# Kernel tuning notes

Measured on AMD Instinct MI355X. Metric: run time of the kernel, lower is better.

The kernel has to match this reference:

```python
import jax, jax.numpy as jnp
import numpy as np

B, N, D, S, ITERS, EPS = 32, 4096, 512, 8, 3, 1e-8


def layer_norm(x, g, b, eps=1e-5):
    mu = jnp.mean(x, axis=-1, keepdims=True)
    var = jnp.var(x, axis=-1, keepdims=True)
    return (x - mu) * jax.lax.rsqrt(var + eps) * g + b


def setup_inputs() -> dict:
    key = jax.random.key(0)
    ks = jax.random.split(key, 12)
    sc = 1.0 / np.sqrt(D)
    return {
        "inputs": jax.random.normal(ks[0], (B, N, D), jnp.float32),
        "noise": jax.random.normal(ks[1], (B, S, D), jnp.float32),
        "slots_mu": jax.random.normal(ks[2], (1, S, D), jnp.float32),
        "slots_sigma": jnp.ones((1, S, D), jnp.float32),
        "ln_in_g": jnp.ones((D,), jnp.float32), "ln_in_b": jnp.zeros((D,), jnp.float32),
        "ln_s_g": jnp.ones((D,), jnp.float32), "ln_s_b": jnp.zeros((D,), jnp.float32),
        "wq": jax.random.normal(ks[3], (D, D), jnp.float32) * sc,
        "wk": jax.random.normal(ks[4], (D, D), jnp.float32) * sc,
        "wv": jax.random.normal(ks[5], (D, D), jnp.float32) * sc,
        "w_ih": jax.random.normal(ks[6], (3 * D, D), jnp.float32) * sc,
        "w_hh": jax.random.normal(ks[7], (3 * D, D), jnp.float32) * sc,
        "b_ih": jnp.zeros((3 * D,), jnp.float32),
        "b_hh": jnp.zeros((3 * D,), jnp.float32),
        "ln_m_g": jnp.ones((D,), jnp.float32), "ln_m_b": jnp.zeros((D,), jnp.float32),
        "w1": jax.random.normal(ks[8], (D, D), jnp.float32) * sc,
        "b1": jnp.zeros((D,), jnp.float32),
        "w2": jax.random.normal(ks[9], (D, D), jnp.float32) * sc,
        "b2": jnp.zeros((D,), jnp.float32),
    }


def reference(inputs, noise, slots_mu, slots_sigma, ln_in_g, ln_in_b, ln_s_g, ln_s_b,
              wq, wk, wv, w_ih, w_hh, b_ih, b_hh, ln_m_g, ln_m_b, w1, b1, w2, b2):
    # slot init: mu + sigma * N(0,1)
    slots = slots_mu + slots_sigma * noise          # (B,S,D)
    x = layer_norm(inputs, ln_in_g, ln_in_b)        # (B,N,D)
    k = jnp.einsum('bnd,ed->bne', x, wk)            # (B,N,D)
    v = jnp.einsum('bnd,ed->bne', x, wv)            # (B,N,D)
    for _ in range(ITERS):
        slots_prev = slots
        sn = layer_norm(slots, ln_s_g, ln_s_b)
        q = jnp.einsum('bsd,ed->bse', sn, wq)       # (B,S,D)
        logits = jnp.einsum('bnd,bsd->bns', k, q)   # (B,N,S)
        attn = jax.nn.softmax(logits, axis=-1) + EPS  # softmax over slots
        attn = attn / jnp.sum(attn, axis=-1, keepdims=True)
        attn_t = jnp.swapaxes(attn, -1, -2)         # (B,S,N)
        updates = jnp.einsum('bsn,bnd->bsd', attn_t, v)
        # GRUCell(input=updates, hidden=slots_prev)
        gi = jnp.einsum('bsd,ed->bse', updates, w_ih) + b_ih
        gh = jnp.einsum('bsd,ed->bse', slots_prev, w_hh) + b_hh
        gi_r, gi_z, gi_n = jnp.split(gi, 3, axis=-1)
        gh_r, gh_z, gh_n = jnp.split(gh, 3, axis=-1)
        r = jax.nn.sigmoid(gi_r + gh_r)
        z = jax.nn.sigmoid(gi_z + gh_z)
        n = jnp.tanh(gi_n + r * gh_n)
        slots = (1.0 - z) * n + z * slots_prev
        # residual MLP
        h = layer_norm(slots, ln_m_g, ln_m_b)
        h = jax.nn.relu(jnp.einsum('bsd,ed->bse', h, w1) + b1)
        slots = slots + jnp.einsum('bsd,ed->bse', h, w2) + b2
    return slots
```

## Files before the change

### kernel.cpp

```cpp
#include <hip/hip_runtime.h>

#define B_ 32
#define N_ 4096
#define D_ 512
#define S_ 8
#define ITERS_ 3
#define CH 32
#define RPC (N_/CH)

__device__ __forceinline__ float sigmoid_f(float x) {
    return 1.0f / (1.0f + __expf(-x));
}
__device__ __forceinline__ float tanh_f(float x) {
    float e = __expf(2.0f * x);
    return 1.0f - 2.0f / (e + 1.0f);
}

__global__ __launch_bounds__(256) void k_init(const float* __restrict__ noise,
                                              const float* __restrict__ mu,
                                              const float* __restrict__ sg,
                                              float* __restrict__ slots,
                                              float* __restrict__ stats) {
    int wid = threadIdx.x >> 6, lane = threadIdx.x & 63;
    int row = blockIdx.x * 4 + wid;
    const float4* nz = (const float4*)(noise + (size_t)row * D_);
    const float4* m4 = (const float4*)(mu + (size_t)(row & 7) * D_);
    const float4* s4 = (const float4*)(sg + (size_t)(row & 7) * D_);
    float4 v0 = nz[lane], v1 = nz[64 + lane];
    float4 a0 = m4[lane], a1 = m4[64 + lane];
    float4 c0 = s4[lane], c1 = s4[64 + lane];
    v0.x = fmaf(c0.x, v0.x, a0.x); v0.y = fmaf(c0.y, v0.y, a0.y);
    v0.z = fmaf(c0.z, v0.z, a0.z); v0.w = fmaf(c0.w, v0.w, a0.w);
    v1.x = fmaf(c1.x, v1.x, a1.x); v1.y = fmaf(c1.y, v1.y, a1.y);
    v1.z = fmaf(c1.z, v1.z, a1.z); v1.w = fmaf(c1.w, v1.w, a1.w);
    float4* o4 = (float4*)(slots + (size_t)row * D_);
    o4[lane] = v0; o4[64 + lane] = v1;
    float s1 = v0.x + v0.y + v0.z + v0.w + v1.x + v1.y + v1.z + v1.w;
    float s2 = v0.x*v0.x; s2 = fmaf(v0.y,v0.y,s2); s2 = fmaf(v0.z,v0.z,s2); s2 = fmaf(v0.w,v0.w,s2);
    s2 = fmaf(v1.x,v1.x,s2); s2 = fmaf(v1.y,v1.y,s2); s2 = fmaf(v1.z,v1.z,s2); s2 = fmaf(v1.w,v1.w,s2);
#pragma unroll
    for (int off = 32; off > 0; off >>= 1) {
        s1 += __shfl_xor(s1, off, 64);
        s2 += __shfl_xor(s2, off, 64);
    }
    if (lane == 0) {
        float mean = s1 * (1.0f / D_);
        float var  = s2 * (1.0f / D_) - mean * mean;
        stats[row * 2]     = mean;
        stats[row * 2 + 1] = rsqrtf(var + 1e-5f);
    }
}

template<int WT, int LNA>
__global__ __launch_bounds__(256) void k_gemm(const float* __restrict__ A,
                                              const float* __restrict__ W,
                                              const float* __restrict__ bias,
                                              const float* __restrict__ resid,
                                              float* __restrict__ C,
                                              int M, int N, int K, int relu,
                                              const float* __restrict__ stats,
                                              const float* __restrict__ lng,
                                              const float* __restrict__ lnb) {
    __shared__ float As[64][68];
    __shared__ float Ws[64][36];
    int t  = threadIdx.x;
    int bm = blockIdx.y * 64, bn = blockIdx.x * 32;
    int tm = t >> 4, tn = t & 15;
    float acc[4][2] = {{0.f,0.f},{0.f,0.f},{0.f,0.f},{0.f,0.f}};

    for (int kk = 0; kk < K; kk += 64) {
        __syncthreads();
        if (WT == 2) {
#pragma unroll
            for (int r = 0; r < 4; ++r) {
                int idx = t + r * 256;
                int k = idx >> 4, m4 = idx & 15;
                float4 a4 = *(const float4*)(A + (size_t)(kk + k) * M + bm + (m4 << 2));
                *(float4*)&As[k][m4 << 2] = a4;
            }
        } else {
#pragma unroll
            for (int r = 0; r < 4; ++r) {
                int flat = t * 4 + r * 1024;
                int m = flat >> 6, k = flat & 63;
                float4 a4 = *(const float4*)(A + (size_t)(bm + m) * K + kk + k);
                if (LNA) {
                    float mean = stats[(bm + m) * 2];
                    float rs   = stats[(bm + m) * 2 + 1];
                    float4 g4 = *(const float4*)(lng + kk + k);
                    float4 b4 = *(const float4*)(lnb + kk + k);
                    a4.x = fmaf((a4.x - mean) * rs, g4.x, b4.x);
                    a4.y = fmaf((a4.y - mean) * rs, g4.y, b4.y);
                    a4.z = fmaf((a4.z - mean) * rs, g4.z, b4.z);
                    a4.w = fmaf((a4.w - mean) * rs, g4.w, b4.w);
                }
                As[k + 0][m] = a4.x; As[k + 1][m] = a4.y;
                As[k + 2][m] = a4.z; As[k + 3][m] = a4.w;
            }
        }
        if (WT == 1) {
#pragma unroll
            for (int r = 0; r < 2; ++r) {
                int flat = t * 4 + r * 1024;
                int n = flat >> 6, k = flat & 63;
                float4 w4 = *(const float4*)(W + (size_t)(bn + n) * K + kk + k);
                Ws[k + 0][n] = w4.x; Ws[k + 1][n] = w4.y;
                Ws[k + 2][n] = w4.z; Ws[k + 3][n] = w4.w;
            }
        } else {
#pragma unroll
            for (int r = 0; r < 2; ++r) {
                int flat = t * 4 + r * 1024;
                int k = flat >> 5, n = flat & 31;
                float4 w4 = *(const float4*)(W + (size_t)(kk + k) * N + bn + n);
                *(float4*)&Ws[k][n] = w4;
            }
        }
        __syncthreads();
#pragma unroll
        for (int k = 0; k < 64; ++k) {
            float4 a = *(const float4*)&As[k][tm << 2];
            float2 w = *(const float2*)&Ws[k][tn << 1];
            acc[0][0] = fmaf(a.x, w.x, acc[0][0]); acc[0][1] = fmaf(a.x, w.y, acc[0][1]);
            acc[1][0] = fmaf(a.y, w.x, acc[1][0]); acc[1][1] = fmaf(a.y, w.y, acc[1][1]);
            acc[2][0] = fmaf(a.z, w.x, acc[2][0]); acc[2][1] = fmaf(a.z, w.y, acc[2][1]);
            acc[3][0] = fmaf(a.w, w.x, acc[3][0]); acc[3][1] = fmaf(a.w, w.y, acc[3][1]);
        }
    }
#pragma unroll
    for (int i = 0; i < 4; ++i) {
#pragma unroll
        for (int j = 0; j < 2; ++j) {
            int row = bm + (tm << 2) + i;
            int col = bn + (tn << 1) + j;
            float v = acc[i][j];
            if (bias)  v += bias[col];
            if (relu)  v = fmaxf(v, 0.0f);
            if (resid) v += resid[(size_t)row * N + col];
            C[(size_t)row * N + col] = v;
        }
    }
}

__global__ __launch_bounds__(256, 2) void k_attn(const float* __restrict__ xin,
                                                 const float* __restrict__ gv,
                                                 const float* __restrict__ bv,
                                                 const float* __restrict__ qk,
                                                 float* __restrict__ part) {
    __shared__ float u0s[S_ * D_];
    const int c = blockIdx.x, b = blockIdx.y;
    const int wid = threadIdx.x >> 6, lane = threadIdx.x & 63;

    float4 qlo[8], qhi[8];
    const float* qb = qk + (size_t)b * S_ * D_;
#pragma unroll
    for (int s = 0; s < 8; ++s) {
        qlo[s] = *(const float4*)(qb + s * 512 + (lane << 2));
        qhi[s] = *(const float4*)(qb + s * 512 + 256 + (lane << 2));
    }
    float4 glo = ((const float4*)gv)[lane], ghi = ((const float4*)gv)[64 + lane];
    float4 blo = ((const float4*)bv)[lane], bhi = ((const float4*)bv)[64 + lane];

    float4 alo[8], ahi[8];
#pragma unroll
    for (int s = 0; s < 8; ++s) {
        alo[s] = make_float4(0.f, 0.f, 0.f, 0.f);
        ahi[s] = make_float4(0.f, 0.f, 0.f, 0.f);
    }
    const float cnorm = 1.0f / (1.0f + 8.0f * 1e-8f);
    const float eadd  = 1e-8f * cnorm;
    const bool hb5 = (lane & 32) != 0, hb4 = (lane & 16) != 0, hb3 = (lane & 8) != 0;
    const int gbase = lane & 7;

    const float* xrow = xin + ((size_t)b * N_ + (size_t)c * RPC + wid) * D_;
    float4 x0lo = ((const float4*)xrow)[lane];
    float4 x0hi = ((const float4*)xrow)[64 + lane];
    const float* xr1 = xrow + 4 * D_;
    float4 x1lo = ((const float4*)xr1)[lane];
    float4 x1hi = ((const float4*)xr1)[64 + lane];

    for (int j = 0; j < RPC / 4; ++j) {
        int jn = (j < RPC / 4 - 2) ? j + 2 : RPC / 4 - 1;
        const float* xn = xrow + (size_t)jn * 4 * D_;
        float4 nlo = ((const float4*)xn)[lane];
        float4 nhi = ((const float4*)xn)[64 + lane];

        float s1 = x0lo.x + x0lo.y + x0lo.z + x0lo.w + x0hi.x + x0hi.y + x0hi.z + x0hi.w;
        float s2 = x0lo.x*x0lo.x; s2 = fmaf(x0lo.y,x0lo.y,s2); s2 = fmaf(x0lo.z,x0lo.z,s2); s2 = fmaf(x0lo.w,x0lo.w,s2);
        s2 = fmaf(x0hi.x,x0hi.x,s2); s2 = fmaf(x0hi.y,x0hi.y,s2); s2 = fmaf(x0hi.z,x0hi.z,s2); s2 = fmaf(x0hi.w,x0hi.w,s2);
#pragma unroll
        for (int off = 32; off > 0; off >>= 1) {
            s1 += __shfl_xor(s1, off, 64);
            s2 += __shfl_xor(s2, off, 64);
        }
        float mean = s1 * (1.0f / D_);
        float var  = s2 * (1.0f / D_) - mean * mean;
        float rs   = rsqrtf(var + 1e-5f);
        float4 hlo, hhi;
        hlo.x = fmaf((x0lo.x - mean) * rs, glo.x, blo.x);
        hlo.y = fmaf((x0lo.y - mean) * rs, glo.y, blo.y);
        hlo.z = fmaf((x0lo.z - mean) * rs, glo.z, blo.z);
        hlo.w = fmaf((x0lo.w - mean) * rs, glo.w, blo.w);
        hhi.x = fmaf((x0hi.x - mean) * rs, ghi.x, bhi.x);
        hhi.y = fmaf((x0hi.y - mean) * rs, ghi.y, bhi.y);
        hhi.z = fmaf((x0hi.z - mean) * rs, ghi.z, bhi.z);
        hhi.w = fmaf((x0hi.w - mean) * rs, ghi.w, bhi.w);

        float dd[8];
#pragma unroll
        for (int s = 0; s < 8; ++s) {
            float td = hlo.x * qlo[s].x;
            td = fmaf(hlo.y, qlo[s].y, td); td = fmaf(hlo.z, qlo[s].z, td); td = fmaf(hlo.w, qlo[s].w, td);
            td = fmaf(hhi.x, qhi[s].x, td); td = fmaf(hhi.y, qhi[s].y, td);
            td = fmaf(hhi.z, qhi[s].z, td); td = fmaf(hhi.w, qhi[s].w, td);
            dd[s] = td;
        }
        float r4[4];
#pragma unroll
        for (int s = 0; s < 4; ++s) {
            float snd = hb5 ? dd[s] : dd[s + 4];
            float kp  = hb5 ? dd[s + 4] : dd[s];
            r4[s] = kp + __shfl_xor(snd, 32, 64);
        }
        float r2[2];
#pragma unroll
        for (int s = 0; s < 2; ++s) {
            float snd = hb4 ? r4[s] : r4[s + 2];
            float kp  = hb4 ? r4[s + 2] : r4[s];
            r2[s] = kp + __shfl_xor(snd, 16, 64);
        }
        float v;
        {
            float snd = hb3 ? r2[0] : r2[1];
            float kp  = hb3 ? r2[1] : r2[0];
            v = kp + __shfl_xor(snd, 8, 64);
        }
        v += __shfl_xor(v, 4, 64);
        v += __shfl_xor(v, 2, 64);
        v += __shfl_xor(v, 1, 64);
        float m = v;
        m = fmaxf(m, __shfl_xor(m, 8, 64));
        m = fmaxf(m, __shfl_xor(m, 16, 64));
        m = fmaxf(m, __shfl_xor(m, 32, 64));
        float p = __expf(v - m);
        float ssum = p;
        ssum += __shfl_xor(ssum, 8, 64);
        ssum += __shfl_xor(ssum, 16, 64);
        ssum += __shfl_xor(ssum, 32, 64);
        float amine = fmaf(p, cnorm / ssum, eadd);
        float av[8];
#pragma unroll
        for (int s = 0; s < 8; ++s) av[s] = __shfl(amine, (s << 3) | gbase, 64);
#pragma unroll
        for (int s = 0; s < 8; ++s) {
            alo[s].x = fmaf(av[s], hlo.x, alo[s].x); alo[s].y = fmaf(av[s], hlo.y, alo[s].y);
            alo[s].z = fmaf(av[s], hlo.z, alo[s].z); alo[s].w = fmaf(av[s], hlo.w, alo[s].w);
            ahi[s].x = fmaf(av[s], hhi.x, ahi[s].x); ahi[s].y = fmaf(av[s], hhi.y, ahi[s].y);
            ahi[s].z = fmaf(av[s], hhi.z, ahi[s].z); ahi[s].w = fmaf(av[s], hhi.w, ahi[s].w);
        }
        x0lo = x1lo; x0hi = x1hi; x1lo = nlo; x1hi = nhi;
    }

    for (int w = 0; w < 4; ++w) {
        if (wid == w) {
#pragma unroll
            for (int s = 0; s < 8; ++s) {
                float* p0 = &u0s[s * 512 + (lane << 2)];
                float* p1 = p0 + 256;
                if (w == 0) {
                    *(float4*)p0 = alo[s];
                    *(float4*)p1 = ahi[s];
                } else {
                    float4 v0 = *(float4*)p0;
                    v0.x += alo[s].x; v0.y += alo[s].y; v0.z += alo[s].z; v0.w += alo[s].w;
                    *(float4*)p0 = v0;
                    float4 v1 = *(float4*)p1;
                    v1.x += ahi[s].x; v1.y += ahi[s].y; v1.z += ahi[s].z; v1.w += ahi[s].w;
                    *(float4*)p1 = v1;
                }
            }
        }
        __syncthreads();
    }
    float4* d4 = (float4*)(part + ((size_t)(b * CH + c)) * (S_ * D_));
    const float4* s4 = (const float4*)u0s;
    for (int i = threadIdx.x; i < 1024; i += 256) d4[i] = s4[i];
}

__global__ void k_reduce_u0(const float* __restrict__ part, float* __restrict__ u0) {
    int i = blockIdx.x * 256 + threadIdx.x;
    int b = i >> 10, r = i & 1023;
    const float4* p4 = (const float4*)part;
    float4 acc = make_float4(0.f, 0.f, 0.f, 0.f);
#pragma unroll
    for (int c = 0; c < CH; ++c) {
        float4 v = p4[(size_t)(b * CH + c) * 1024 + r];
        acc.x += v.x; acc.y += v.y; acc.z += v.z; acc.w += v.w;
    }
    ((float4*)u0)[i] = acc;
}

__global__ __launch_bounds__(512) void k_p2(const float* __restrict__ gi,
                                            const float* __restrict__ gh,
                                            const float* __restrict__ slots,
                                            const float* __restrict__ w1, const float* __restrict__ b1,
                                            const float* __restrict__ w2, const float* __restrict__ b2,
                                            const float* __restrict__ wqkT,
                                            const float* __restrict__ ln_m_g, const float* __restrict__ ln_m_b,
                                            const float* __restrict__ ln_s_g, const float* __restrict__ ln_s_b,
                                            float* __restrict__ dst, float* __restrict__ qkout, int last) {
    __shared__ float s2s[2][512];
    __shared__ float t0s[2][512];
    __shared__ float hs[2][512];
    __shared__ float stat[4];
    const int t = threadIdx.x;
    const int wid = t >> 6, lane = t & 63;
    const int r0 = blockIdx.x * 2;

#pragma unroll
    for (int j = 0; j < 2; ++j) {
        int flat = t + j * 512;
        int r = flat >> 9, d = flat & 511;
        size_t row = r0 + r;
        const float* gib = gi + row * 1536;
        const float* ghb = gh + row * 1536;
        float gir = gib[d], giz = gib[d + 512], gin = gib[d + 1024];
        float ghr = ghb[d], ghz = ghb[d + 512], ghn = ghb[d + 1024];
        float rr = sigmoid_f(gir + ghr);
        float zz = sigmoid_f(giz + ghz);
        float nn = tanh_f(fmaf(rr, ghn, gin));
        float sp = slots[row * 512 + d];
        s2s[r][d] = fmaf(1.0f - zz, nn, zz * sp);
    }
    __syncthreads();
    if (wid < 2) {
        const float4* sr = (const float4*)s2s[wid];
        float4 a = sr[lane], bq = sr[64 + lane];
        float s1 = a.x + a.y + a.z + a.w + bq.x + bq.y + bq.z + bq.w;
        float s2 = a.x*a.x; s2 = fmaf(a.y,a.y,s2); s2 = fmaf(a.z,a.z,s2); s2 = fmaf(a.w,a.w,s2);
        s2 = fmaf(bq.x,bq.x,s2); s2 = fmaf(bq.y,bq.y,s2); s2 = fmaf(bq.z,bq.z,s2); s2 = fmaf(bq.w,bq.w,s2);
#pragma unroll
        for (int off = 32; off > 0; off >>= 1) {
            s1 += __shfl_xor(s1, off, 64);
            s2 += __shfl_xor(s2, off, 64);
        }
        if (lane == 0) {
            float mean = s1 * (1.0f / D_);
            float var  = s2 * (1.0f / D_) - mean * mean;
            stat[wid * 2] = mean;
            stat[wid * 2 + 1] = rsqrtf(var + 1e-5f);
        }
    }
    __syncthreads();
#pragma unroll
    for (int j = 0; j < 2; ++j) {
        int flat = t + j * 512;
        int r = flat >> 9, d = flat & 511;
        t0s[r][d] = fmaf((s2s[r][d] - stat[r * 2]) * stat[r * 2 + 1], ln_m_g[d], ln_m_b[d]);
    }
    __syncthreads();
    {
        const int c = t;
        const float4* wr = (const float4*)(w1 + (size_t)c * 512);
        float a0 = 0.f, a1 = 0.f;
#pragma unroll 8
        for (int k4 = 0; k4 < 128; ++k4) {
            float4 w4 = wr[k4];
            float4 q0 = *(const float4*)&t0s[0][k4 << 2];
            float4 q1 = *(const float4*)&t0s[1][k4 << 2];
            a0 = fmaf(q0.x, w4.x, a0); a0 = fmaf(q0.y, w4.y, a0);
            a0 = fmaf(q0.z, w4.z, a0); a0 = fmaf(q0.w, w4.w, a0);
            a1 = fmaf(q1.x, w4.x, a1); a1 = fmaf(q1.y, w4.y, a1);
            a1 = fmaf(q1.z, w4.z, a1); a1 = fmaf(q1.w, w4.w, a1);
        }
        float bc = b1[c];
        hs[0][c] = fmaxf(a0 + bc, 0.f);
        hs[1][c] = fmaxf(a1 + bc, 0.f);
    }
    __syncthreads();
    {
        const int c = t;
        const float4* wr = (const float4*)(w2 + (size_t)c * 512);
        float a0 = 0.f, a1 = 0.f;
#pragma unroll 8
        for (int k4 = 0; k4 < 128; ++k4) {
            float4 w4 = wr[k4];
            float4 q0 = *(const float4*)&hs[0][k4 << 2];
            float4 q1 = *(const float4*)&hs[1][k4 << 2];
            a0 = fmaf(q0.x, w4.x, a0); a0 = fmaf(q0.y, w4.y, a0);
            a0 = fmaf(q0.z, w4.z, a0); a0 = fmaf(q0.w, w4.w, a0);
            a1 = fmaf(q1.x, w4.x, a1); a1 = fmaf(q1.y, w4.y, a1);
            a1 = fmaf(q1.z, w4.z, a1); a1 = fmaf(q1.w, w4.w, a1);
        }
        float bc = b2[c];
        float o0 = s2s[0][c] + a0 + bc;
        float o1 = s2s[1][c] + a1 + bc;
        dst[(size_t)r0 * 512 + c] = o0;
        dst[(size_t)(r0 + 1) * 512 + c] = o1;
        s2s[0][c] = o0;
        s2s[1][c] = o1;
    }
    if (last) return;
    __syncthreads();
    if (wid < 2) {
        const float4* sr = (const float4*)s2s[wid];
        float4 a = sr[lane], bq = sr[64 + lane];
        float s1 = a.x + a.y + a.z + a.w + bq.x + bq.y + bq.z + bq.w;
        float s2 = a.x*a.x; s2 = fmaf(a.y,a.y,s2); s2 = fmaf(a.z,a.z,s2); s2 = fmaf(a.w,a.w,s2);
        s2 = fmaf(bq.x,bq.x,s2); s2 = fmaf(bq.y,bq.y,s2); s2 = fmaf(bq.z,bq.z,s2); s2 = fmaf(bq.w,bq.w,s2);
#pragma unroll
        for (int off = 32; off > 0; off >>= 1) {
            s1 += __shfl_xor(s1, off, 64);
            s2 += __shfl_xor(s2, off, 64);
        }
        if (lane == 0) {
            float mean = s1 * (1.0f / D_);
            float var  = s2 * (1.0f / D_) - mean * mean;
            stat[wid * 2] = mean;
            stat[wid * 2 + 1] = rsqrtf(var + 1e-5f);
        }
    }
    __syncthreads();
#pragma unroll
    for (int j = 0; j < 2; ++j) {
        int flat = t + j * 512;
        int r = flat >> 9, d = flat & 511;
        t0s[r][d] = fmaf((s2s[r][d] - stat[r * 2]) * stat[r * 2 + 1], ln_s_g[d], ln_s_b[d]);
    }
    __syncthreads();
    {
        const int c = t;
        const float4* wr = (const float4*)(wqkT + (size_t)c * 512);
        float a0 = 0.f, a1 = 0.f;
#pragma unroll 8
        for (int k4 = 0; k4 < 128; ++k4) {
            float4 w4 = wr[k4];
            float4 q0 = *(const float4*)&t0s[0][k4 << 2];
            float4 q1 = *(const float4*)&t0s[1][k4 << 2];
            a0 = fmaf(q0.x, w4.x, a0); a0 = fmaf(q0.y, w4.y, a0);
            a0 = fmaf(q0.z, w4.z, a0); a0 = fmaf(q0.w, w4.w, a0);
            a1 = fmaf(q1.x, w4.x, a1); a1 = fmaf(q1.y, w4.y, a1);
            a1 = fmaf(q1.z, w4.z, a1); a1 = fmaf(q1.w, w4.w, a1);
        }
        qkout[(size_t)r0 * 512 + c] = a0;
        qkout[(size_t)(r0 + 1) * 512 + c] = a1;
    }
}

extern "C" void kernel_launch(void* const* d_in, const int* in_sizes, int n_in,
                              void* d_out, int out_size, void* d_ws, size_t ws_size,
                              hipStream_t stream) {
    const float* inputs  = (const float*)d_in[0];
    const float* noise   = (const float*)d_in[1];
    const float* mu      = (const float*)d_in[2];
    const float* sg      = (const float*)d_in[3];
    const float* ln_in_g = (const float*)d_in[4];
    const float* ln_in_b = (const float*)d_in[5];
    const float* ln_s_g  = (const float*)d_in[6];
    const float* ln_s_b  = (const float*)d_in[7];
    const float* wq      = (const float*)d_in[8];
    const float* wk      = (const float*)d_in[9];
    const float* wv      = (const float*)d_in[10];
    const float* w_ih    = (const float*)d_in[11];
    const float* w_hh    = (const float*)d_in[12];
    const float* b_ih    = (const float*)d_in[13];
    const float* b_hh    = (const float*)d_in[14];
    const float* ln_m_g  = (const float*)d_in[15];
    const float* ln_m_b  = (const float*)d_in[16];
    const float* w1      = (const float*)d_in[17];
    const float* b1      = (const float*)d_in[18];
    const float* w2      = (const float*)d_in[19];
    const float* b2      = (const float*)d_in[20];

    float* ws = (float*)d_ws;
    const size_t SLOT = (size_t)B_ * S_ * D_;
    float* slots = ws;
    float* qk    = ws + SLOT;
    float* u0    = ws + 2 * SLOT;
    float* upd   = ws + 3 * SLOT;
    float* gi    = ws + 4 * SLOT;
    float* gh    = gi + 3 * SLOT;
    float* wqkT  = gh + 3 * SLOT;
    float* stats = wqkT + 2 * SLOT;
    float* part  = stats + 1024;

    k_gemm<2,0><<<dim3(16, 8), 256, 0, stream>>>(wk, wq, nullptr, nullptr, wqkT,
                                                 512, 512, 512, 0, nullptr, nullptr, nullptr);
    k_init<<<64, 256, 0, stream>>>(noise, mu, sg, slots, stats);
    k_gemm<1,1><<<dim3(16, 4), 256, 0, stream>>>(slots, wqkT, nullptr, nullptr, qk,
                                                 256, 512, 512, 0, stats, ln_s_g, ln_s_b);

    for (int it = 0; it < ITERS_; ++it) {
        k_attn<<<dim3(CH, B_), 256, 0, stream>>>(inputs, ln_in_g, ln_in_b, qk, part);
        k_reduce_u0<<<128, 256, 0, stream>>>(part, u0);
        k_gemm<1,0><<<dim3(16, 4), 256, 0, stream>>>(u0, wv, nullptr, nullptr, upd,
                                                     256, 512, 512, 0, nullptr, nullptr, nullptr);
        k_gemm<1,0><<<dim3(48, 4), 256, 0, stream>>>(upd, w_ih, b_ih, nullptr, gi,
                                                     256, 1536, 512, 0, nullptr, nullptr, nullptr);
        k_gemm<1,0><<<dim3(48, 4), 256, 0, stream>>>(slots, w_hh, b_hh, nullptr, gh,
                                                     256, 1536, 512, 0, nullptr, nullptr, nullptr);
        int last = (it == ITERS_ - 1);
        float* dst = last ? (float*)d_out : slots;
        k_p2<<<128, 512, 0, stream>>>(gi, gh, slots, w1, b1, w2, b2, wqkT,
                                      ln_m_g, ln_m_b, ln_s_g, ln_s_b, dst, qk, last);
    }
}
```

Measured before the change: 812.6 us.

## Split attention into logits and weighted-sum kernels with algebraic layernorm folding

Result: slower. 857.2 us (+5.5%).

```diff
diff --git a/kernel.cpp b/kernel.cpp
--- a/kernel.cpp
+++ b/kernel.cpp
@@ -5,8 +5,6 @@
 #define D_ 512
 #define S_ 8
 #define ITERS_ 3
-#define CH 32
-#define RPC (N_/CH)
 
 __device__ __forceinline__ float sigmoid_f(float x) {
     return 1.0f / (1.0f + __expf(-x));
@@ -142,162 +140,178 @@
     }
 }
 
-__global__ __launch_bounds__(256, 2) void k_attn(const float* __restrict__ xin,
-                                                 const float* __restrict__ gv,
-                                                 const float* __restrict__ bv,
-                                                 const float* __restrict__ qk,
-                                                 float* __restrict__ part) {
-    __shared__ float u0s[S_ * D_];
-    const int c = blockIdx.x, b = blockIdx.y;
-    const int wid = threadIdx.x >> 6, lane = threadIdx.x & 63;
-
-    float4 qlo[8], qhi[8];
-    const float* qb = qk + (size_t)b * S_ * D_;
-#pragma unroll
-    for (int s = 0; s < 8; ++s) {
-        qlo[s] = *(const float4*)(qb + s * 512 + (lane << 2));
-        qhi[s] = *(const float4*)(qb + s * 512 + 256 + (lane << 2));
-    }
-    float4 glo = ((const float4*)gv)[lane], ghi = ((const float4*)gv)[64 + lane];
-    float4 blo = ((const float4*)bv)[lane], bhi = ((const float4*)bv)[64 + lane];
-
-    float4 alo[8], ahi[8];
-#pragma unroll
-    for (int s = 0; s < 8; ++s) {
-        alo[s] = make_float4(0.f, 0.f, 0.f, 0.f);
-        ahi[s] = make_float4(0.f, 0.f, 0.f, 0.f);
-    }
+__global__ __launch_bounds__(256) void k_qprep(const float* __restrict__ qk,
+                                               const float* __restrict__ g,
+                                               const float* __restrict__ bvec,
+                                               float* __restrict__ qt,
+                                               float* __restrict__ c12) {
+    __shared__ float qts[4096];
+    __shared__ float qks[4096];
+    int b = blockIdx.x, t = threadIdx.x;
+    const float4* src = (const float4*)(qk + (size_t)b * 4096);
+    const float4* g4  = (const float4*)g;
+    float4* qtg = (float4*)(qt + (size_t)b * 4096);
+#pragma unroll
+    for (int r = 0; r < 4; ++r) {
+        int f = t + r * 256;
+        float4 v  = src[f];
+        float4 gg = g4[f & 127];
+        float4 qv = make_float4(v.x*gg.x, v.y*gg.y, v.z*gg.z, v.w*gg.w);
+        *(float4*)&qts[f * 4] = qv;
+        *(float4*)&qks[f * 4] = v;
+        qtg[(f & 127) * 8 + (f >> 7)] = qv;
+    }
+    __syncthreads();
+    int s = t >> 5, j = t & 31;
+    float c1p = 0.f, c2p = 0.f;
+#pragma unroll 4
+    for (int e = 0; e < 16; ++e) {
+        int d = j + 32 * e;
+        c1p += qts[s * 512 + d];
+        c2p = fmaf(bvec[d], qks[s * 512 + d], c2p);
+    }
+#pragma unroll
+    for (int off = 16; off > 0; off >>= 1) {
+        c1p += __shfl_xor(c1p, off, 64);
+        c2p += __shfl_xor(c2p, off, 64);
+    }
+    if (j == 0) { c12[b * 16 + s] = c1p; c12[b * 16 + 8 + s] = c2p; }
+}
+
+__global__ __launch_bounds__(256) void k_attnA(const float* __restrict__ x,
+                                               const float* __restrict__ qt,
+                                               const float* __restrict__ c12,
+                                               float* __restrict__ wa,
+                                               float* __restrict__ murs) {
+    const int b = blockIdx.y;
+    const int n = blockIdx.x * 256 + threadIdx.x;
+    const size_t gr = (size_t)b * N_ + n;
+    const float4* rp = (const float4*)(x + gr * D_);
+    const float4* qp = (const float4*)(qt + (size_t)b * 4096);
+
+    float dot[8] = {0.f,0.f,0.f,0.f,0.f,0.f,0.f,0.f};
+    float sx = 0.f, sxx = 0.f;
+#pragma unroll 4
+    for (int k4 = 0; k4 < 128; ++k4) {
+        float4 xv = rp[k4];
+        sx += xv.x + xv.y + xv.z + xv.w;
+        sxx = fmaf(xv.x, xv.x, sxx); sxx = fmaf(xv.y, xv.y, sxx);
+        sxx = fmaf(xv.z, xv.z, sxx); sxx = fmaf(xv.w, xv.w, sxx);
+#pragma unroll
+        for (int s = 0; s < 8; ++s) {
+            float4 qv = qp[k4 * 8 + s];
+            dot[s] = fmaf(xv.x, qv.x, dot[s]);
+            dot[s] = fmaf(xv.y, qv.y, dot[s]);
+            dot[s] = fmaf(xv.z, qv.z, dot[s]);
+            dot[s] = fmaf(xv.w, qv.w, dot[s]);
+        }
+    }
+    float mean = sx * (1.0f / D_);
+    float rs   = rsqrtf(sxx * (1.0f / D_) - mean * mean + 1e-5f);
+    float mc   = -rs * mean;
+    float l[8];
+#pragma unroll
+    for (int s = 0; s < 8; ++s)
+        l[s] = fmaf(rs, dot[s], fmaf(mc, c12[b * 16 + s], c12[b * 16 + 8 + s]));
+    float mx = l[0];
+#pragma unroll
+    for (int s = 1; s < 8; ++s) mx = fmaxf(mx, l[s]);
+    float p[8], psum = 0.f;
+#pragma unroll
+    for (int s = 0; s < 8; ++s) { p[s] = __expf(l[s] - mx); psum += p[s]; }
     const float cnorm = 1.0f / (1.0f + 8.0f * 1e-8f);
     const float eadd  = 1e-8f * cnorm;
-    const bool hb5 = (lane & 32) != 0, hb4 = (lane & 16) != 0, hb3 = (lane & 8) != 0;
-    const int gbase = lane & 7;
-
-    const float* xrow = xin + ((size_t)b * N_ + (size_t)c * RPC + wid) * D_;
-    float4 x0lo = ((const float4*)xrow)[lane];
-    float4 x0hi = ((const float4*)xrow)[64 + lane];
-    const float* xr1 = xrow + 4 * D_;
-    float4 x1lo = ((const float4*)xr1)[lane];
-    float4 x1hi = ((const float4*)xr1)[64 + lane];
-
-    for (int j = 0; j < RPC / 4; ++j) {
-        int jn = (j < RPC / 4 - 2) ? j + 2 : RPC / 4 - 1;
-        const float* xn = xrow + (size_t)jn * 4 * D_;
-        float4 nlo = ((const float4*)xn)[lane];
-        float4 nhi = ((const float4*)xn)[64 + lane];
-
-        float s1 = x0lo.x + x0lo.y + x0lo.z + x0lo.w + x0hi.x + x0hi.y + x0hi.z + x0hi.w;
-        float s2 = x0lo.x*x0lo.x; s2 = fmaf(x0lo.y,x0lo.y,s2); s2 = fmaf(x0lo.z,x0lo.z,s2); s2 = fmaf(x0lo.w,x0lo.w,s2);
-        s2 = fmaf(x0hi.x,x0hi.x,s2); s2 = fmaf(x0hi.y,x0hi.y,s2); s2 = fmaf(x0hi.z,x0hi.z,s2); s2 = fmaf(x0hi.w,x0hi.w,s2);
-#pragma unroll
-        for (int off = 32; off > 0; off >>= 1) {
-            s1 += __shfl_xor(s1, off, 64);
-            s2 += __shfl_xor(s2, off, 64);
-        }
-        float mean = s1 * (1.0f / D_);
-        float var  = s2 * (1.0f / D_) - mean * mean;
-        float rs   = rsqrtf(var + 1e-5f);
-        float4 hlo, hhi;
-        hlo.x = fmaf((x0lo.x - mean) * rs, glo.x, blo.x);
-        hlo.y = fmaf((x0lo.y - mean) * rs, glo.y, blo.y);
-        hlo.z = fmaf((x0lo.z - mean) * rs, glo.z, blo.z);
-        hlo.w = fmaf((x0lo.w - mean) * rs, glo.w, blo.w);
-        hhi.x = fmaf((x0hi.x - mean) * rs, ghi.x, bhi.x);
-        hhi.y = fmaf((x0hi.y - mean) * rs, ghi.y, bhi.y);
-        hhi.z = fmaf((x0hi.z - mean) * rs, ghi.z, bhi.z);
-        hhi.w = fmaf((x0hi.w - mean) * rs, ghi.w, bhi.w);
-
-        float dd[8];
-#pragma unroll
-        for (int s = 0; s < 8; ++s) {
-            float td = hlo.x * qlo[s].x;
-            td = fmaf(hlo.y, qlo[s].y, td); td = fmaf(hlo.z, qlo[s].z, td); td = fmaf(hlo.w, qlo[s].w, td);
-            td = fmaf(hhi.x, qhi[s].x, td); td = fmaf(hhi.y, qhi[s].y, td);
-            td = fmaf(hhi.z, qhi[s].z, td); td = fmaf(hhi.w, qhi[s].w, td);
-            dd[s] = td;
-        }
-        float r4[4];
-#pragma unroll
-        for (int s = 0; s < 4; ++s) {
-            float snd = hb5 ? dd[s] : dd[s + 4];
-            float kp  = hb5 ? dd[s + 4] : dd[s];
-            r4[s] = kp + __shfl_xor(snd, 32, 64);
-        }
-        float r2[2];
-#pragma unroll
-        for (int s = 0; s < 2; ++s) {
-            float snd = hb4 ? r4[s] : r4[s + 2];
-            float kp  = hb4 ? r4[s + 2] : r4[s];
-            r2[s] = kp + __shfl_xor(snd, 16, 64);
-        }
-        float v;
-        {
-            float snd = hb3 ? r2[0] : r2[1];
-            float kp  = hb3 ? r2[1] : r2[0];
-            v = kp + __shfl_xor(snd, 8, 64);
-        }
-        v += __shfl_xor(v, 4, 64);
-        v += __shfl_xor(v, 2, 64);
-        v += __shfl_xor(v, 1, 64);
-        float m = v;
-        m = fmaxf(m, __shfl_xor(m, 8, 64));
-        m = fmaxf(m, __shfl_xor(m, 16, 64));
-        m = fmaxf(m, __shfl_xor(m, 32, 64));
-        float p = __expf(v - m);
-        float ssum = p;
-        ssum += __shfl_xor(ssum, 8, 64);
-        ssum += __shfl_xor(ssum, 16, 64);
-        ssum += __shfl_xor(ssum, 32, 64);
-        float amine = fmaf(p, cnorm / ssum, eadd);
-        float av[8];
-#pragma unroll
-        for (int s = 0; s < 8; ++s) av[s] = __shfl(amine, (s << 3) | gbase, 64);
-#pragma unroll
-        for (int s = 0; s < 8; ++s) {
-            alo[s].x = fmaf(av[s], hlo.x, alo[s].x); alo[s].y = fmaf(av[s], hlo.y, alo[s].y);
-            alo[s].z = fmaf(av[s], hlo.z, alo[s].z); alo[s].w = fmaf(av[s], hlo.w, alo[s].w);
-            ahi[s].x = fmaf(av[s], hhi.x, ahi[s].x); ahi[s].y = fmaf(av[s], hhi.y, ahi[s].y);
-            ahi[s].z = fmaf(av[s], hhi.z, ahi[s].z); ahi[s].w = fmaf(av[s], hhi.w, ahi[s].w);
-        }
-        x0lo = x1lo; x0hi = x1hi; x1lo = nlo; x1hi = nhi;
-    }
-
-    for (int w = 0; w < 4; ++w) {
-        if (wid == w) {
-#pragma unroll
-            for (int s = 0; s < 8; ++s) {
-                float* p0 = &u0s[s * 512 + (lane << 2)];
-                float* p1 = p0 + 256;
-                if (w == 0) {
-                    *(float4*)p0 = alo[s];
-                    *(float4*)p1 = ahi[s];
-                } else {
-                    float4 v0 = *(float4*)p0;
-                    v0.x += alo[s].x; v0.y += alo[s].y; v0.z += alo[s].z; v0.w += alo[s].w;
-                    *(float4*)p0 = v0;
-                    float4 v1 = *(float4*)p1;
-                    v1.x += ahi[s].x; v1.y += ahi[s].y; v1.z += ahi[s].z; v1.w += ahi[s].w;
-                    *(float4*)p1 = v1;
-                }
-            }
+    float ip = cnorm / psum;
+    float a[8], w[8];
+#pragma unroll
+    for (int s = 0; s < 8; ++s) { a[s] = fmaf(p[s], ip, eadd); w[s] = a[s] * rs; }
+    float4* wo = (float4*)(wa + gr * 16);
+    wo[0] = make_float4(w[0], w[1], w[2], w[3]);
+    wo[1] = make_float4(w[4], w[5], w[6], w[7]);
+    wo[2] = make_float4(a[0], a[1], a[2], a[3]);
+    wo[3] = make_float4(a[4], a[5], a[6], a[7]);
+    ((float2*)murs)[gr] = make_float2(mean, rs);
+}
+
+__global__ __launch_bounds__(256) void k_attnB(const float* __restrict__ x,
+                                               const float* __restrict__ wa,
+                                               float* __restrict__ part) {
+    const int b = blockIdx.y, nc = blockIdx.x, t = threadIdx.x;
+    const int d0 = t * 2;
+    const float*  xp = x  + ((size_t)b * N_ + (size_t)nc * 256) * D_ + d0;
+    const float4* wp = (const float4*)(wa + ((size_t)b * N_ + (size_t)nc * 256) * 16);
+    float P[8][2];
+#pragma unroll
+    for (int s = 0; s < 8; ++s) { P[s][0] = 0.f; P[s][1] = 0.f; }
+#pragma unroll 4
+    for (int i = 0; i < 256; ++i) {
+        float2 xv = *(const float2*)(xp + (size_t)i * D_);
+        float4 w01 = wp[i * 4];
+        float4 w23 = wp[i * 4 + 1];
+        P[0][0] = fmaf(w01.x, xv.x, P[0][0]); P[0][1] = fmaf(w01.x, xv.y, P[0][1]);
+        P[1][0] = fmaf(w01.y, xv.x, P[1][0]); P[1][1] = fmaf(w01.y, xv.y, P[1][1]);
+        P[2][0] = fmaf(w01.z, xv.x, P[2][0]); P[2][1] = fmaf(w01.z, xv.y, P[2][1]);
+        P[3][0] = fmaf(w01.w, xv.x, P[3][0]); P[3][1] = fmaf(w01.w, xv.y, P[3][1]);
+        P[4][0] = fmaf(w23.x, xv.x, P[4][0]); P[4][1] = fmaf(w23.x, xv.y, P[4][1]);
+        P[5][0] = fmaf(w23.y, xv.x, P[5][0]); P[5][1] = fmaf(w23.y, xv.y, P[5][1]);
+        P[6][0] = fmaf(w23.z, xv.x, P[6][0]); P[6][1] = fmaf(w23.z, xv.y, P[6][1]);
+        P[7][0] = fmaf(w23.w, xv.x, P[7][0]); P[7][1] = fmaf(w23.w, xv.y, P[7][1]);
+    }
+    float* o = part + (size_t)(b * 16 + nc) * 4096;
+#pragma unroll
+    for (int s = 0; s < 8; ++s)
+        *(float2*)(o + s * 512 + d0) = make_float2(P[s][0], P[s][1]);
+}
+
+__global__ __launch_bounds__(256) void k_ured(const float* __restrict__ part,
+                                              const float* __restrict__ wa,
+                                              const float* __restrict__ murs,
+                                              const float* __restrict__ g,
+                                              const float* __restrict__ bvec,
+                                              float* __restrict__ u0) {
+    __shared__ float red[256][16];
+    const int b = blockIdx.x, t = threadIdx.x;
+    float aA[8] = {0,0,0,0,0,0,0,0}, aT[8] = {0,0,0,0,0,0,0,0};
+    const float4* wp = (const float4*)(wa + (size_t)b * N_ * 16);
+    const float2* mp = ((const float2*)murs) + (size_t)b * N_;
+    for (int i = t; i < N_; i += 256) {
+        float4 w01 = wp[i * 4], w23 = wp[i * 4 + 1];
+        float4 a01 = wp[i * 4 + 2], a23 = wp[i * 4 + 3];
+        float mu = mp[i].x;
+        aA[0] += a01.x; aA[1] += a01.y; aA[2] += a01.z; aA[3] += a01.w;
+        aA[4] += a23.x; aA[5] += a23.y; aA[6] += a23.z; aA[7] += a23.w;
+        aT[0] = fmaf(w01.x, mu, aT[0]); aT[1] = fmaf(w01.y, mu, aT[1]);
+        aT[2] = fmaf(w01.z, mu, aT[2]); aT[3] = fmaf(w01.w, mu, aT[3]);
+        aT[4] = fmaf(w23.x, mu, aT[4]); aT[5] = fmaf(w23.y, mu, aT[5]);
+        aT[6] = fmaf(w23.z, mu, aT[6]); aT[7] = fmaf(w23.w, mu, aT[7]);
+    }
+#pragma unroll
+    for (int q = 0; q < 8; ++q) { red[t][q] = aA[q]; red[t][8 + q] = aT[q]; }
+    __syncthreads();
+    for (int step = 128; step > 0; step >>= 1) {
+        if (t < step) {
+#pragma unroll
+            for (int q = 0; q < 16; ++q) red[t][q] += red[t + step][q];
         }
         __syncthreads();
     }
-    float4* d4 = (float4*)(part + ((size_t)(b * CH + c)) * (S_ * D_));
-    const float4* s4 = (const float4*)u0s;
-    for (int i = threadIdx.x; i < 1024; i += 256) d4[i] = s4[i];
-}
-
-__global__ void k_reduce_u0(const float* __restrict__ part, float* __restrict__ u0) {
-    int i = blockIdx.x * 256 + threadIdx.x;
-    int b = i >> 10, r = i & 1023;
-    const float4* p4 = (const float4*)part;
-    float4 acc = make_float4(0.f, 0.f, 0.f, 0.f);
-#pragma unroll
-    for (int c = 0; c < CH; ++c) {
-        float4 v = p4[(size_t)(b * CH + c) * 1024 + r];
-        acc.x += v.x; acc.y += v.y; acc.z += v.z; acc.w += v.w;
-    }
-    ((float4*)u0)[i] = acc;
+    float Av[8], Tv[8];
+#pragma unroll
+    for (int q = 0; q < 8; ++q) { Av[q] = red[0][q]; Tv[q] = red[0][8 + q]; }
+    const int d0 = t * 2;
+    float gg0 = g[d0], gg1 = g[d0 + 1], bb0 = bvec[d0], bb1 = bvec[d0 + 1];
+#pragma unroll
+    for (int s = 0; s < 8; ++s) {
+        float p0 = 0.f, p1 = 0.f;
+#pragma unroll
+        for (int nc = 0; nc < 16; ++nc) {
+            float2 pv = *(const float2*)(part + (size_t)(b * 16 + nc) * 4096 + s * 512 + d0);
+            p0 += pv.x; p1 += pv.y;
+        }
+        float* o = u0 + (size_t)(b * 8 + s) * D_ + d0;
+        o[0] = fmaf(gg0, p0 - Tv[s], Av[s] * bb0);
+        o[1] = fmaf(gg1, p1 - Tv[s], Av[s] * bb1);
+    }
 }
 
 __global__ __launch_bounds__(512) void k_p2(const float* __restrict__ gi,
@@ -474,34 +488,41 @@
 
     float* ws = (float*)d_ws;
     const size_t SLOT = (size_t)B_ * S_ * D_;
-    float* slots = ws;
-    float* qk    = ws + SLOT;
-    float* u0    = ws + 2 * SLOT;
-    float* upd   = ws + 3 * SLOT;
-    float* gi    = ws + 4 * SLOT;
-    float* gh    = gi + 3 * SLOT;
-    float* wqkT  = gh + 3 * SLOT;
-    float* stats = wqkT + 2 * SLOT;
-    float* part  = stats + 1024;
-
-    k_gemm<2,0><<<dim3(16, 8), 256, 0, stream>>>(wk, wq, nullptr, nullptr, wqkT,
+    size_t o = 0;
+    float* slots = ws + o; o += SLOT;
+    float* qk    = ws + o; o += SLOT;
+    float* u0    = ws + o; o += SLOT;
+    float* gi    = ws + o; o += 3 * SLOT;
+    float* gh    = ws + o; o += 3 * SLOT;
+    float* Mqk   = ws + o; o += (size_t)D_ * D_;
+    float* Wiv   = ws + o; o += (size_t)3 * D_ * D_;
+    float* statsS= ws + o; o += 512;
+    float* qt    = ws + o; o += SLOT;
+    float* c12   = ws + o; o += 512;
+    float* murs  = ws + o; o += (size_t)2 * B_ * N_;
+    float* wa    = ws + o; o += (size_t)16 * B_ * N_;
+    float* part  = ws + o; o += (size_t)16 * B_ * 4096;
+
+    k_gemm<2,0><<<dim3(16, 8), 256, 0, stream>>>(wk, wq, nullptr, nullptr, Mqk,
                                                  512, 512, 512, 0, nullptr, nullptr, nullptr);
-    k_init<<<64, 256, 0, stream>>>(noise, mu, sg, slots, stats);
-    k_gemm<1,1><<<dim3(16, 4), 256, 0, stream>>>(slots, wqkT, nullptr, nullptr, qk,
-                                                 256, 512, 512, 0, stats, ln_s_g, ln_s_b);
+    k_gemm<0,0><<<dim3(16, 24), 256, 0, stream>>>(w_ih, wv, nullptr, nullptr, Wiv,
+                                                  1536, 512, 512, 0, nullptr, nullptr, nullptr);
+    k_init<<<64, 256, 0, stream>>>(noise, mu, sg, slots, statsS);
+    k_gemm<1,1><<<dim3(16, 4), 256, 0, stream>>>(slots, Mqk, nullptr, nullptr, qk,
+                                                 256, 512, 512, 0, statsS, ln_s_g, ln_s_b);
 
     for (int it = 0; it < ITERS_; ++it) {
-        k_attn<<<dim3(CH, B_), 256, 0, stream>>>(inputs, ln_in_g, ln_in_b, qk, part);
-        k_reduce_u0<<<128, 256, 0, stream>>>(part, u0);
-        k_gemm<1,0><<<dim3(16, 4), 256, 0, stream>>>(u0, wv, nullptr, nullptr, upd,
-                                                     256, 512, 512, 0, nullptr, nullptr, nullptr);
-        k_gemm<1,0><<<dim3(48, 4), 256, 0, stream>>>(upd, w_ih, b_ih, nullptr, gi,
+        k_qprep<<<B_, 256, 0, stream>>>(qk, ln_in_g, ln_in_b, qt, c12);
+        k_attnA<<<dim3(16, B_), 256, 0, stream>>>(inputs, qt, c12, wa, murs);
+        k_attnB<<<dim3(16, B_), 256, 0, stream>>>(inputs, wa, part);
+        k_ured<<<B_, 256, 0, stream>>>(part, wa, murs, ln_in_g, ln_in_b, u0);
+        k_gemm<1,0><<<dim3(48, 4), 256, 0, stream>>>(slots, w_hh, b_hh, nullptr, gh,
                                                      256, 1536, 512, 0, nullptr, nullptr, nullptr);
-        k_gemm<1,0><<<dim3(48, 4), 256, 0, stream>>>(slots, w_hh, b_hh, nullptr, gh,
+        k_gemm<1,0><<<dim3(48, 4), 256, 0, stream>>>(u0, Wiv, b_ih, nullptr, gi,
                                                      256, 1536, 512, 0, nullptr, nullptr, nullptr);
         int last = (it == ITERS_ - 1);
         float* dst = last ? (float*)d_out : slots;
-        k_p2<<<128, 512, 0, stream>>>(gi, gh, slots, w1, b1, w2, b2, wqkT,
+        k_p2<<<128, 512, 0, stream>>>(gi, gh, slots, w1, b1, w2, b2, Mqk,
                                       ln_m_g, ln_m_b, ln_s_g, ln_s_b, dst, qk, last);
     }
 }
```
